# Optimization experiments

Hardware: AMD Instinct MI355X
Metric: run time of the kernel (lower is better)

The kernel has to match this reference:

```python
import jax, jax.numpy as jnp
from jax import lax
import numpy as np

KS = 3          # kernel_size
PAD = 1         # padding of conv_offset
N = KS * KS     # sampling points per pixel
B, C, H, W = 8, 64, 96, 96
OUTC = 64


def setup_inputs() -> dict:
    key = jax.random.key(0)
    k1, k2, k3 = jax.random.split(key, 3)
    x = jax.random.normal(k1, (B, C, H, W), dtype=jnp.float32)
    # conv_offset: Conv2d(C, 2N, ks=3, pad=1); small init so offsets are modest
    w_off = jax.random.normal(k2, (2 * N, C, KS, KS), dtype=jnp.float32) * 0.01
    b_off = jnp.zeros((2 * N,), jnp.float32)
    # conv_kernel: Conv2d(C, OUTC, ks=3, stride=3)
    w_ker = jax.random.normal(k3, (OUTC, C, KS, KS), dtype=jnp.float32) * (1.0 / np.sqrt(C * KS * KS))
    b_ker = jnp.zeros((OUTC,), jnp.float32)
    return {"x": x, "w_off": w_off, "b_off": b_off, "w_ker": w_ker, "b_ker": b_ker}


def _deform_conv(x, w_off, b_off, w_ker, b_ker):
    b, c, h, w = x.shape
    dn = ('NCHW', 'OIHW', 'NCHW')
    # offset field: (b, 2N, h, w); channels [:N] are x(row) offsets, [N:] are y(col)
    offset = lax.conv_general_dilated(x, w_off, (1, 1), [(PAD, PAD), (PAD, PAD)],
                                      dimension_numbers=dn) + b_off[None, :, None, None]
    r = jnp.arange(-(KS - 1) // 2, (KS - 1) // 2 + 1)
    pnx, pny = jnp.meshgrid(r, r, indexing='ij')          # kernel grid offsets p_n
    gx, gy = jnp.meshgrid(jnp.arange(h), jnp.arange(w), indexing='ij')  # p_0
    px = gx[None, None].astype(x.dtype) + pnx.reshape(1, N, 1, 1).astype(x.dtype) + offset[:, :N]
    py = gy[None, None].astype(x.dtype) + pny.reshape(1, N, 1, 1).astype(x.dtype) + offset[:, N:]
    # Bilinear sampling with zero outside the grid. This is exactly the dense
    # G @ x of the original (only the 4 neighbors of p have nonzero G weight).
    x0 = jnp.floor(px); y0 = jnp.floor(py)
    lx = px - x0; ly = py - y0            # grads flow to offsets through lx/ly
    x0i = lax.stop_gradient(x0).astype(jnp.int32)
    y0i = lax.stop_gradient(y0).astype(jnp.int32)
    x_flat = x.transpose(0, 2, 3, 1).reshape(b, h * w, c)  # (b, HW, c)

    def corner(xi, yi, wt):
        valid = ((xi >= 0) & (xi < h) & (yi >= 0) & (yi < w)).astype(x.dtype)
        idx = (jnp.clip(xi, 0, h - 1) * w + jnp.clip(yi, 0, w - 1)).reshape(b, -1)
        g = jax.vmap(lambda im, ix: im[ix])(x_flat, idx)   # (b, N*h*w, c)
        return g * (wt * valid).reshape(b, -1, 1)

    val = (corner(x0i,     y0i,     (1 - lx) * (1 - ly))
           + corner(x0i + 1, y0i,     lx * (1 - ly))
           + corner(x0i,     y0i + 1, (1 - lx) * ly)
           + corner(x0i + 1, y0i + 1, lx * ly))            # (b, N*h*w, c)
    xo = val.reshape(b, N, h, w, c).transpose(0, 4, 2, 3, 1)        # (b,c,h,w,N)
    # _reshape_x_offset: N -> (kr,kc) tiled into (h*ks, w*ks)
    xo = xo.reshape(b, c, h, w, KS, KS).transpose(0, 1, 2, 4, 3, 5).reshape(b, c, h * KS, w * KS)
    out = lax.conv_general_dilated(xo, w_ker, (KS, KS), 'VALID',
                                   dimension_numbers=dn) + b_ker[None, :, None, None]
    return out  # (b, OUTC, h, w)


def reference(x, w_off, b_off, w_ker, b_ker):
    return _deform_conv(x, w_off, b_off, w_ker, b_ker)
```

## Files before the change

### kernel.cpp

```cpp
#include <hip/hip_runtime.h>

#define H_ 96
#define W_ 96
#define HW 9216
#define C_ 64
#define OUTC 64
#define NPTS 9
#define NCH 18
#define B_ 8
#define NPIX 73728

#define PCH 72

typedef __attribute__((ext_vector_type(8))) short short8;
typedef __attribute__((ext_vector_type(4))) float f32x4;
typedef __attribute__((ext_vector_type(4))) unsigned int uint4v;

__device__ __forceinline__ short f2bf(float f) {
    union { float f; unsigned u; } v; v.f = f;
    unsigned r = v.u + 0x7fffu + ((v.u >> 16) & 1u);
    return (short)(r >> 16);
}
__device__ __forceinline__ float bflo(unsigned d) {
    union { unsigned u; float f; } v; v.u = d << 16; return v.f;
}
__device__ __forceinline__ float bfhi(unsigned d) {
    union { unsigned u; float f; } v; v.u = d & 0xffff0000u; return v.f;
}

__global__ __launch_bounds__(256) void prep_xpose(
    const float* __restrict__ x, const float* __restrict__ w_ker,
    const float* __restrict__ w_off, short* __restrict__ x_t,
    short* __restrict__ wk_frag, short* __restrict__ woff_frag)
{
    int blk = blockIdx.x;
    int t   = threadIdx.x;
    if (blk < 1152) {
        int b   = blk & 7;
        int sub = blk >> 3;
        int cb  = t & 7;
        int pix = (sub * 32 + (t >> 3)) * 2;

        const float* xp = x + ((size_t)(b * C_ + cb * 8) * HW) + pix;
        float tl[8][2];
#pragma unroll
        for (int e = 0; e < 8; ++e) {
            float2 v = *(const float2*)(xp + (size_t)e * HW);
            tl[e][0] = v.x; tl[e][1] = v.y;
        }
#pragma unroll
        for (int p = 0; p < 2; ++p) {
            short8 s;
#pragma unroll
            for (int e = 0; e < 8; ++e) s[e] = f2bf(tl[e][p]);
            *(short8*)(x_t + ((size_t)(b * HW + pix + p) * 64) + cb * 8) = s;
        }
    } else {
        int idx = (blk - 1152) * 256 + t;
        if (idx < 36864) {
            int j = idx & 7, l = (idx >> 3) & 63, nt = (idx >> 9) & 3, sg = idx >> 11;
            int q2 = sg & 1, n = sg >> 1;
            int c  = q2 * 32 + ((l >> 4) << 3) + j;
            int oc = nt * 16 + (l & 15);
            wk_frag[idx] = f2bf(w_ker[(oc * C_ + c) * 9 + n]);
        } else {
            int k = idx - 36864;
            int j = k & 7, l = (k >> 3) & 63, nt = (k >> 9) & 1, sg = k >> 10;
            int q2 = sg & 1, n = sg >> 1;
            int c  = q2 * 32 + ((l >> 4) << 3) + j;
            int oc = nt * 16 + (l & 15);
            woff_frag[k] = (oc < NCH) ? f2bf(w_off[(oc * C_ + c) * 9 + n]) : (short)0;
        }
    }
}

__global__ __launch_bounds__(128, 3) void deform_fused(
    const short* __restrict__ x_t, const short* __restrict__ woff_frag,
    const float* __restrict__ b_off, const short* __restrict__ wk_frag,
    const float* __restrict__ b_ker, float* __restrict__ out)
{
    __shared__ short  sX[100 * PCH];
    __shared__ float  sE[64 * 20];
    __shared__ float2 sP[16 * 9];

    int t    = threadIdx.x;
    int lane = t & 63;
    int wv   = t >> 6;
    int b    = blockIdx.x & 7;
    int strip= blockIdx.x >> 3;
    int px0  = strip * 16;
    int i    = px0 / W_;
    int j0   = px0 - i * W_;
    int pxl  = lane & 15, kq = lane >> 4;
    int j    = j0 + pxl;
    const short* xb = x_t + (size_t)b * HW * 64;
    const short8 Z8 = {0,0,0,0,0,0,0,0};

    for (int u = t; u < 800; u += 128) {
        int cb = u & 7, rc = u >> 3;
        int r = rc / 20, c = rc - r * 20;
        int row = min(max(i - 2 + r, 0), H_ - 1);
        int col = min(max(j0 - 2 + c, 0), W_ - 1);
        *(short8*)&sX[rc * PCH + cb * 8] =
            *(const short8*)(xb + (row * W_ + col) * 64 + cb * 8);
    }
    __syncthreads();

    f32x4 pa0 = {0,0,0,0}, pa1 = {0,0,0,0};
    auto p1tap = [&](int n) {
        int di = n / 3 - 1, dj = n % 3 - 1;
        int ii = i + di, jj = j + dj;
        bool ok = (ii >= 0) & (ii < H_) & (jj >= 0) & (jj < W_);
        int rc = (di + 2) * 20 + (pxl + dj + 2);
#pragma unroll
        for (int q2 = 0; q2 < 2; ++q2) {
            short8 a = *(const short8*)&sX[rc * PCH + q2 * 32 + kq * 8];
            a = ok ? a : Z8;
            const short* wb = woff_frag + ((n * 2 + q2) * 2) * 512 + lane * 8;
            short8 b0 = *(const short8*)(wb);
            short8 b1 = *(const short8*)(wb + 512);
            pa0 = __builtin_amdgcn_mfma_f32_16x16x32_bf16(a, b0, pa0, 0, 0, 0);
            pa1 = __builtin_amdgcn_mfma_f32_16x16x32_bf16(a, b1, pa1, 0, 0, 0);
        }
    };
    if (wv == 0) {
#pragma unroll
        for (int q = 0; q < 5; ++q) p1tap(q);
    } else {
#pragma unroll
        for (int q = 0; q < 4; ++q) p1tap(5 + q);
    }
    {
        int col = lane & 15, rq = lane >> 4;
#pragma unroll
        for (int r = 0; r < 4; ++r)
            sE[(wv * 16 + rq * 4 + r) * 20 + col] = pa0[r];
        if (col < 2) {
#pragma unroll
            for (int r = 0; r < 4; ++r)
                sE[(wv * 16 + rq * 4 + r) * 20 + 16 + col] = pa1[r];
        }
    }
    __syncthreads();

#pragma unroll
    for (int s = 0; s < 2; ++s) {
        int idx = s * 128 + t;
        if (idx < 144) {
            int p = idx / 9, n = idx - p * 9;
            float ox = sE[p * 20 + n]     + sE[(16 + p) * 20 + n]     + b_off[n];
            float oy = sE[p * 20 + 9 + n] + sE[(16 + p) * 20 + 9 + n] + b_off[9 + n];
            sP[p * 9 + n] = make_float2(ox, oy);
        }
    }
    __syncthreads();

    f32x4 acc[4];
#pragma unroll
    for (int nt = 0; nt < 4; ++nt) acc[nt] = (f32x4){0.f, 0.f, 0.f, 0.f};

    auto p2tap = [&](int n) {
        int di = n / 3 - 1, dj = n % 3 - 1;
        float2 o = sP[pxl * 9 + n];
        float fpx = (float)(i + di) + o.x;
        float fpy = (float)(j + dj) + o.y;
        float x0f = floorf(fpx), y0f = floorf(fpy);
        float lx = fpx - x0f, ly = fpy - y0f;
        int xi = (int)x0f, yi = (int)y0f;
        float wx0 = (xi >= 0  && xi <= H_ - 1) ? (1.0f - lx) : 0.0f;
        float wx1 = (xi >= -1 && xi <= H_ - 2) ? lx          : 0.0f;
        float wy0 = (yi >= 0  && yi <= W_ - 1) ? (1.0f - ly) : 0.0f;
        float wy1 = (yi >= -1 && yi <= W_ - 2) ? ly          : 0.0f;
        float w00 = wx0 * wy0, w10 = wx1 * wy0, w01 = wx0 * wy1, w11 = wx1 * wy1;
        int rp = xi - (i - 2), cp = yi - (j0 - 2);
        bool inp = (rp >= 0) & (rp <= 3) & (cp >= 0) & (cp <= 18);
        uint4v u[8];
        if (inp) {
            int l00 = (rp * 20 + cp) * PCH;
            int l10 = l00 + 20 * PCH, l01 = l00 + PCH, l11 = l10 + PCH;
#pragma unroll
            for (int q2 = 0; q2 < 2; ++q2) {
                int cho = q2 * 32 + kq * 8;
                u[q2*4+0] = *(const uint4v*)&sX[l00 + cho];
                u[q2*4+1] = *(const uint4v*)&sX[l10 + cho];
                u[q2*4+2] = *(const uint4v*)&sX[l01 + cho];
                u[q2*4+3] = *(const uint4v*)&sX[l11 + cho];
            }
        }
        if (!inp) {
            int r0 = min(max(xi,     0), H_ - 1) * W_;
            int r1 = min(max(xi + 1, 0), H_ - 1) * W_;
            int c0 = min(max(yi,     0), W_ - 1);
            int c1 = min(max(yi + 1, 0), W_ - 1);
#pragma unroll
            for (int q2 = 0; q2 < 2; ++q2) {
                int cho = q2 * 32 + kq * 8;
                u[q2*4+0] = *(const uint4v*)(xb + (r0 + c0) * 64 + cho);
                u[q2*4+1] = *(const uint4v*)(xb + (r1 + c0) * 64 + cho);
                u[q2*4+2] = *(const uint4v*)(xb + (r0 + c1) * 64 + cho);
                u[q2*4+3] = *(const uint4v*)(xb + (r1 + c1) * 64 + cho);
            }
        }
#pragma unroll
        for (int q2 = 0; q2 < 2; ++q2) {
            short8 A;
#pragma unroll
            for (int d = 0; d < 4; ++d) {
                float lo = w00 * bflo(u[q2*4+0][d]) + w10 * bflo(u[q2*4+1][d])
                         + w01 * bflo(u[q2*4+2][d]) + w11 * bflo(u[q2*4+3][d]);
                float hi = w00 * bfhi(u[q2*4+0][d]) + w10 * bfhi(u[q2*4+1][d])
                         + w01 * bfhi(u[q2*4+2][d]) + w11 * bfhi(u[q2*4+3][d]);
                A[2 * d]     = f2bf(lo);
                A[2 * d + 1] = f2bf(hi);
            }
            const short* wbp = wk_frag + ((n * 2 + q2) * 4) * 512 + lane * 8;
#pragma unroll
            for (int nt = 0; nt < 4; ++nt) {
                short8 bfr = *(const short8*)(wbp + nt * 512);
                acc[nt] = __builtin_amdgcn_mfma_f32_16x16x32_bf16(A, bfr, acc[nt], 0, 0, 0);
            }
        }
    };
    if (wv == 0) {
#pragma unroll
        for (int q = 0; q < 4; ++q) p2tap(q);
    } else {
#pragma unroll
        for (int q = 0; q < 5; ++q) p2tap(4 + q);
    }

    __syncthreads();
    int col = lane & 15, rq = lane >> 4;
    if (wv == 0) {
#pragma unroll
        for (int nt = 0; nt < 4; ++nt) {
            int oc = nt * 16 + col;
            float bias = b_ker[oc];
#pragma unroll
            for (int r = 0; r < 4; ++r)
                sE[oc * 20 + rq * 4 + r] = acc[nt][r] + bias;
        }
    }
    __syncthreads();
    if (wv == 1) {
#pragma unroll
        for (int nt = 0; nt < 4; ++nt) {
            int oc = nt * 16 + col;
#pragma unroll
            for (int r = 0; r < 4; ++r)
                sE[oc * 20 + rq * 4 + r] += acc[nt][r];
        }
    }
    __syncthreads();

    int oc = t >> 1, half = t & 1;
    const float* se = &sE[oc * 20 + half * 8];
    float* outp = out + ((size_t)(b * OUTC + oc) * HW) + px0 + half * 8;
    *(f32x4*)outp       = *(const f32x4*)se;
    *(f32x4*)(outp + 4) = *(const f32x4*)(se + 4);
}

extern "C" void kernel_launch(void* const* d_in, const int* in_sizes, int n_in,
                              void* d_out, int out_size, void* d_ws, size_t ws_size,
                              hipStream_t stream) {
    const float* x     = (const float*)d_in[0];
    const float* w_off = (const float*)d_in[1];
    const float* b_off = (const float*)d_in[2];
    const float* w_ker = (const float*)d_in[3];
    const float* b_ker = (const float*)d_in[4];
    float* out = (float*)d_out;

    char*  wsb       = (char*)d_ws;
    short* x_t       = (short*)wsb;
    short* wk_frag   = (short*)(wsb + 9437184);
    short* woff_frag = wk_frag + 36864;

    prep_xpose  <<<1368, 256, 0, stream>>>(x, w_ker, w_off, x_t, wk_frag, woff_frag);
    deform_fused<<<4608, 128, 0, stream>>>(x_t, woff_frag, b_off, wk_frag, b_ker, out);
}
```

Before: 113.9 us.

## Drop NHWC bf16 transpose pass; read fp32 NCHW input directly in fused kernel

```diff
diff --git a/kernel.cpp b/kernel.cpp
--- a/kernel.cpp
+++ b/kernel.cpp
@@ -21,6 +21,12 @@
     unsigned r = v.u + 0x7fffu + ((v.u >> 16) & 1u);
     return (short)(r >> 16);
 }
+__device__ __forceinline__ unsigned pack2bf(float lo, float hi) {
+    union { float f; unsigned u; } a, b2; a.f = lo; b2.f = hi;
+    unsigned ra = (a.u  + 0x7fffu + ((a.u  >> 16) & 1u)) >> 16;
+    unsigned rb = (b2.u + 0x7fffu + ((b2.u >> 16) & 1u)) & 0xffff0000u;
+    return (ra & 0xffffu) | rb;
+}
 __device__ __forceinline__ float bflo(unsigned d) {
     union { unsigned u; float f; } v; v.u = d << 16; return v.f;
 }
@@ -28,58 +34,33 @@
     union { unsigned u; float f; } v; v.u = d & 0xffff0000u; return v.f;
 }
 
-__global__ __launch_bounds__(256) void prep_xpose(
-    const float* __restrict__ x, const float* __restrict__ w_ker,
-    const float* __restrict__ w_off, short* __restrict__ x_t,
+__global__ __launch_bounds__(256) void prep_w(
+    const float* __restrict__ w_ker, const float* __restrict__ w_off,
     short* __restrict__ wk_frag, short* __restrict__ woff_frag)
 {
-    int blk = blockIdx.x;
-    int t   = threadIdx.x;
-    if (blk < 1152) {
-        int b   = blk & 7;
-        int sub = blk >> 3;
-        int cb  = t & 7;
-        int pix = (sub * 32 + (t >> 3)) * 2;
-
-        const float* xp = x + ((size_t)(b * C_ + cb * 8) * HW) + pix;
-        float tl[8][2];
-#pragma unroll
-        for (int e = 0; e < 8; ++e) {
-            float2 v = *(const float2*)(xp + (size_t)e * HW);
-            tl[e][0] = v.x; tl[e][1] = v.y;
-        }
-#pragma unroll
-        for (int p = 0; p < 2; ++p) {
-            short8 s;
-#pragma unroll
-            for (int e = 0; e < 8; ++e) s[e] = f2bf(tl[e][p]);
-            *(short8*)(x_t + ((size_t)(b * HW + pix + p) * 64) + cb * 8) = s;
-        }
+    int idx = blockIdx.x * 256 + threadIdx.x;
+    if (idx < 36864) {
+        int j = idx & 7, l = (idx >> 3) & 63, nt = (idx >> 9) & 3, sg = idx >> 11;
+        int q2 = sg & 1, n = sg >> 1;
+        int c  = q2 * 32 + ((l >> 4) << 3) + j;
+        int oc = nt * 16 + (l & 15);
+        wk_frag[idx] = f2bf(w_ker[(oc * C_ + c) * 9 + n]);
     } else {
-        int idx = (blk - 1152) * 256 + t;
-        if (idx < 36864) {
-            int j = idx & 7, l = (idx >> 3) & 63, nt = (idx >> 9) & 3, sg = idx >> 11;
-            int q2 = sg & 1, n = sg >> 1;
-            int c  = q2 * 32 + ((l >> 4) << 3) + j;
-            int oc = nt * 16 + (l & 15);
-            wk_frag[idx] = f2bf(w_ker[(oc * C_ + c) * 9 + n]);
-        } else {
-            int k = idx - 36864;
-            int j = k & 7, l = (k >> 3) & 63, nt = (k >> 9) & 1, sg = k >> 10;
-            int q2 = sg & 1, n = sg >> 1;
-            int c  = q2 * 32 + ((l >> 4) << 3) + j;
-            int oc = nt * 16 + (l & 15);
-            woff_frag[k] = (oc < NCH) ? f2bf(w_off[(oc * C_ + c) * 9 + n]) : (short)0;
-        }
+        int k = idx - 36864;
+        int j = k & 7, l = (k >> 3) & 63, nt = (k >> 9) & 1, sg = k >> 10;
+        int q2 = sg & 1, n = sg >> 1;
+        int c  = q2 * 32 + ((l >> 4) << 3) + j;
+        int oc = nt * 16 + (l & 15);
+        woff_frag[k] = (oc < NCH) ? f2bf(w_off[(oc * C_ + c) * 9 + n]) : (short)0;
     }
 }
 
 __global__ __launch_bounds__(128, 3) void deform_fused(
-    const short* __restrict__ x_t, const short* __restrict__ woff_frag,
+    const float* __restrict__ x, const short* __restrict__ woff_frag,
     const float* __restrict__ b_off, const short* __restrict__ wk_frag,
     const float* __restrict__ b_ker, float* __restrict__ out)
 {
-    __shared__ short  sX[100 * PCH];
+    __shared__ __align__(16) short sX[100 * PCH];
     __shared__ float  sE[64 * 20];
     __shared__ float2 sP[16 * 9];
 
@@ -93,7 +74,7 @@
     int j0   = px0 - i * W_;
     int pxl  = lane & 15, kq = lane >> 4;
     int j    = j0 + pxl;
-    const short* xb = x_t + (size_t)b * HW * 64;
+    const float* xb = x + (size_t)b * C_ * HW;
     const short8 Z8 = {0,0,0,0,0,0,0,0};
 
     for (int u = t; u < 800; u += 128) {
@@ -101,8 +82,11 @@
         int r = rc / 20, c = rc - r * 20;
         int row = min(max(i - 2 + r, 0), H_ - 1);
         int col = min(max(j0 - 2 + c, 0), W_ - 1);
-        *(short8*)&sX[rc * PCH + cb * 8] =
-            *(const short8*)(xb + (row * W_ + col) * 64 + cb * 8);
+        const float* xsrc = xb + (size_t)(cb * 8) * HW + row * W_ + col;
+        short8 s;
+#pragma unroll
+        for (int e = 0; e < 8; ++e) s[e] = f2bf(xsrc[(size_t)e * HW]);
+        *(short8*)&sX[rc * PCH + cb * 8] = s;
     }
     __syncthreads();
 
@@ -194,11 +178,16 @@
             int c1 = min(max(yi + 1, 0), W_ - 1);
 #pragma unroll
             for (int q2 = 0; q2 < 2; ++q2) {
-                int cho = q2 * 32 + kq * 8;
-                u[q2*4+0] = *(const uint4v*)(xb + (r0 + c0) * 64 + cho);
-                u[q2*4+1] = *(const uint4v*)(xb + (r1 + c0) * 64 + cho);
-                u[q2*4+2] = *(const uint4v*)(xb + (r0 + c1) * 64 + cho);
-                u[q2*4+3] = *(const uint4v*)(xb + (r1 + c1) * 64 + cho);
+#pragma unroll
+                for (int d = 0; d < 4; ++d) {
+                    int c = q2 * 32 + kq * 8 + d * 2;
+                    const float* xc0 = xb + (size_t)c * HW;
+                    const float* xc1 = xc0 + HW;
+                    u[q2*4+0][d] = pack2bf(xc0[r0 + c0], xc1[r0 + c0]);
+                    u[q2*4+1][d] = pack2bf(xc0[r1 + c0], xc1[r1 + c0]);
+                    u[q2*4+2][d] = pack2bf(xc0[r0 + c1], xc1[r0 + c1]);
+                    u[q2*4+3][d] = pack2bf(xc0[r1 + c1], xc1[r1 + c1]);
+                }
             }
         }
 #pragma unroll
@@ -270,11 +259,9 @@
     const float* b_ker = (const float*)d_in[4];
     float* out = (float*)d_out;
 
-    char*  wsb       = (char*)d_ws;
-    short* x_t       = (short*)wsb;
-    short* wk_frag   = (short*)(wsb + 9437184);
+    short* wk_frag   = (short*)d_ws;
     short* woff_frag = wk_frag + 36864;
 
-    prep_xpose  <<<1368, 256, 0, stream>>>(x, w_ker, w_off, x_t, wk_frag, woff_frag);
-    deform_fused<<<4608, 128, 0, stream>>>(x_t, woff_frag, b_off, wk_frag, b_ker, out);
-}
+    prep_w      <<<216,  256, 0, stream>>>(w_ker, w_off, wk_frag, woff_frag);
+    deform_fused<<<4608, 128, 0, stream>>>(x, woff_frag, b_off, wk_frag, b_ker, out);
+}
```

Measured after the change: 124.7 us. 9.5% more time.

## Split taps across four waves per block instead of two

Applied to the files above, without the earlier changes.

```diff
diff --git a/kernel.cpp b/kernel.cpp
--- a/kernel.cpp
+++ b/kernel.cpp
@@ -74,12 +74,12 @@
     }
 }
 
-__global__ __launch_bounds__(128, 3) void deform_fused(
+__global__ __launch_bounds__(256, 6) void deform_fused(
     const short* __restrict__ x_t, const short* __restrict__ woff_frag,
     const float* __restrict__ b_off, const short* __restrict__ wk_frag,
     const float* __restrict__ b_ker, float* __restrict__ out)
 {
-    __shared__ short  sX[100 * PCH];
+    __shared__ __align__(16) short sX[100 * PCH];
     __shared__ float  sE[64 * 20];
     __shared__ float2 sP[16 * 9];
 
@@ -96,7 +96,7 @@
     const short* xb = x_t + (size_t)b * HW * 64;
     const short8 Z8 = {0,0,0,0,0,0,0,0};
 
-    for (int u = t; u < 800; u += 128) {
+    for (int u = t; u < 800; u += 256) {
         int cb = u & 7, rc = u >> 3;
         int r = rc / 20, c = rc - r * 20;
         int row = min(max(i - 2 + r, 0), H_ - 1);
@@ -123,13 +123,10 @@
             pa1 = __builtin_amdgcn_mfma_f32_16x16x32_bf16(a, b1, pa1, 0, 0, 0);
         }
     };
-    if (wv == 0) {
-#pragma unroll
-        for (int q = 0; q < 5; ++q) p1tap(q);
-    } else {
-#pragma unroll
-        for (int q = 0; q < 4; ++q) p1tap(5 + q);
-    }
+    if      (wv == 0) { p1tap(0); p1tap(1); }
+    else if (wv == 1) { p1tap(2); p1tap(3); }
+    else if (wv == 2) { p1tap(4); p1tap(5); }
+    else              { p1tap(6); p1tap(7); p1tap(8); }
     {
         int col = lane & 15, rq = lane >> 4;
 #pragma unroll
@@ -143,15 +140,13 @@
     }
     __syncthreads();
 
-#pragma unroll
-    for (int s = 0; s < 2; ++s) {
-        int idx = s * 128 + t;
-        if (idx < 144) {
-            int p = idx / 9, n = idx - p * 9;
-            float ox = sE[p * 20 + n]     + sE[(16 + p) * 20 + n]     + b_off[n];
-            float oy = sE[p * 20 + 9 + n] + sE[(16 + p) * 20 + 9 + n] + b_off[9 + n];
-            sP[p * 9 + n] = make_float2(ox, oy);
-        }
+    if (t < 144) {
+        int p = t / 9, n = t - p * 9;
+        float ox = sE[p * 20 + n]             + sE[(16 + p) * 20 + n]
+                 + sE[(32 + p) * 20 + n]      + sE[(48 + p) * 20 + n]      + b_off[n];
+        float oy = sE[p * 20 + 9 + n]         + sE[(16 + p) * 20 + 9 + n]
+                 + sE[(32 + p) * 20 + 9 + n]  + sE[(48 + p) * 20 + 9 + n]  + b_off[9 + n];
+        sP[p * 9 + n] = make_float2(ox, oy);
     }
     __syncthreads();
 
@@ -221,13 +216,10 @@
             }
         }
     };
-    if (wv == 0) {
-#pragma unroll
-        for (int q = 0; q < 4; ++q) p2tap(q);
-    } else {
-#pragma unroll
-        for (int q = 0; q < 5; ++q) p2tap(4 + q);
-    }
+    if      (wv == 0) { p2tap(0); p2tap(1); }
+    else if (wv == 1) { p2tap(2); p2tap(3); }
+    else if (wv == 2) { p2tap(4); p2tap(5); }
+    else              { p2tap(6); p2tap(7); p2tap(8); }
 
     __syncthreads();
     int col = lane & 15, rq = lane >> 4;
@@ -252,12 +244,32 @@
         }
     }
     __syncthreads();
-
-    int oc = t >> 1, half = t & 1;
-    const float* se = &sE[oc * 20 + half * 8];
-    float* outp = out + ((size_t)(b * OUTC + oc) * HW) + px0 + half * 8;
-    *(f32x4*)outp       = *(const f32x4*)se;
-    *(f32x4*)(outp + 4) = *(const f32x4*)(se + 4);
+    if (wv == 2) {
+#pragma unroll
+        for (int nt = 0; nt < 4; ++nt) {
+            int oc = nt * 16 + col;
+#pragma unroll
+            for (int r = 0; r < 4; ++r)
+                sE[oc * 20 + rq * 4 + r] += acc[nt][r];
+        }
+    }
+    __syncthreads();
+    if (wv == 3) {
+#pragma unroll
+        for (int nt = 0; nt < 4; ++nt) {
+            int oc = nt * 16 + col;
+#pragma unroll
+            for (int r = 0; r < 4; ++r)
+                sE[oc * 20 + rq * 4 + r] += acc[nt][r];
+        }
+    }
+    __syncthreads();
+
+    int oc = t >> 2, qr = t & 3;
+    const float* se = &sE[oc * 20 + qr * 4];
+    float* outp = out + ((size_t)(b * OUTC + oc) * HW) + px0 + qr * 4;
+    *(f32x4*)outp = *(const f32x4*)se;
+
 }
 
 extern "C" void kernel_launch(void* const* d_in, const int* in_sizes, int n_in,
@@ -276,5 +288,5 @@
     short* woff_frag = wk_frag + 36864;
 
     prep_xpose  <<<1368, 256, 0, stream>>>(x, w_ker, w_off, x_t, wk_frag, woff_frag);
-    deform_fused<<<4608, 128, 0, stream>>>(x_t, woff_frag, b_off, wk_frag, b_ker, out);
-}
+    deform_fused<<<4608, 256, 0, stream>>>(x_t, woff_frag, b_off, wk_frag, b_ker, out);
+}
```

Result: faster. 111.4 us (-2.2%).
